# Optimization experiments

Measured on AMD Instinct MI355X. Metric: run time of the kernel, lower is better.

The kernel has to match this reference:

```python
import math
import jax, jax.numpy as jnp
import numpy as np

N_QUBITS = 8
N_QLAYERS = 2
HIDDEN = 768
BATCH = 8192
LN_EPS = 1e-5


def _ry_gate(theta):
    # theta: scalar or (B,) -> (2,2) or (B,2,2) complex64
    h = theta * 0.5
    c, s = jnp.cos(h), jnp.sin(h)
    g = jnp.stack([jnp.stack([c, -s], axis=-1), jnp.stack([s, c], axis=-1)], axis=-2)
    return g.astype(jnp.complex64)


def _rz_gate(theta):
    t = theta.astype(jnp.complex64)
    e0, e1 = jnp.exp(-0.5j * t), jnp.exp(0.5j * t)
    z = jnp.zeros_like(e0)
    return jnp.stack([jnp.stack([e0, z], axis=-1), jnp.stack([z, e1], axis=-1)], axis=-2)


def _apply_1q(state, gate, w, n):
    # state: (B, 2**n); gate: (2,2) shared or (B,2,2) per-sample; wire w (0 = MSB)
    B = state.shape[0]
    s = state.reshape(B, 2 ** w, 2, -1)
    if gate.ndim == 2:
        s = jnp.einsum('ij,bljr->blir', gate, s)
    else:
        s = jnp.einsum('bij,bljr->blir', gate, s)
    return s.reshape(B, -1)


def _apply_cnot(state, c, t, n):
    B = state.shape[0]
    s = state.reshape((B,) + (2,) * n)
    ax_c = 1 + c
    s0 = jnp.take(s, 0, axis=ax_c)  # control=0 branch, control axis removed
    s1 = jnp.take(s, 1, axis=ax_c)
    ax_t = 1 + t - (1 if t > c else 0)
    s1 = jnp.flip(s1, axis=ax_t)    # X on target when control=1
    s = jnp.stack([s0, s1], axis=ax_c)
    return s.reshape(B, -1)


def _circuit(angles, weights_ry, weights_rz):
    # angles: (B, n) float32 -> (B, n) PauliZ expectations, batched statevector sim
    n, L = N_QUBITS, N_QLAYERS
    B = angles.shape[0]
    state = jnp.zeros((B, 2 ** n), dtype=jnp.complex64).at[:, 0].set(1.0)
    for i in range(n):
        state = _apply_1q(state, _ry_gate(angles[:, i]), i, n)
    for i in range(1, n):
        state = _apply_cnot(state, 0, i, n)
    for l in range(L):
        for i in range(n):
            state = _apply_1q(state, _ry_gate(weights_ry[l, i]), i, n)
            state = _apply_1q(state, _rz_gate(weights_rz[l, i]), i, n)
    for i in range(1, n):
        state = _apply_cnot(state, i, 0, n)
    probs = jnp.abs(state) ** 2  # (B, 2**n)
    k = jnp.arange(2 ** n)
    bits = (k[None, :] >> (n - 1 - jnp.arange(n))[:, None]) & 1  # wire 0 = MSB (PennyLane)
    signs = (1 - 2 * bits).astype(probs.dtype)  # (n, 2**n)
    return probs @ signs.T  # (B, n)


def setup_inputs() -> dict:
    key = jax.random.key(0)
    ks = jax.random.split(key, 8)
    return {
        'hidden': jax.random.normal(ks[0], (BATCH, HIDDEN), dtype=jnp.float32),
        'W_in': jax.random.normal(ks[1], (N_QUBITS, HIDDEN), dtype=jnp.float32) * (1.0 / math.sqrt(HIDDEN)),
        'b_in': jax.random.normal(ks[2], (N_QUBITS,), dtype=jnp.float32) * 0.01,
        'W_out': jax.random.normal(ks[3], (HIDDEN, N_QUBITS), dtype=jnp.float32) * (1.0 / math.sqrt(N_QUBITS)),
        'b_out': jax.random.normal(ks[4], (HIDDEN,), dtype=jnp.float32) * 0.01,
        'weights_ry': jax.random.normal(ks[5], (N_QLAYERS, N_QUBITS), dtype=jnp.float32) * 0.1,
        'weights_rz': jax.random.normal(ks[6], (N_QLAYERS, N_QUBITS), dtype=jnp.float32) * 0.1,
        'gamma': jnp.ones((HIDDEN,), dtype=jnp.float32),
        'beta': jnp.zeros((HIDDEN,), dtype=jnp.float32),
    }


def reference(hidden, W_in, b_in, W_out, b_out, weights_ry, weights_rz, gamma, beta):
    phase = 0.0
    angles = jnp.tanh(hidden @ W_in.T + b_in) * math.pi + phase  # (B, n)
    meas = _circuit(angles, weights_ry, weights_rz).astype(jnp.float32)  # (B, n)
    y = meas @ W_out.T + b_out  # (B, h)
    mu = jnp.mean(y, axis=-1, keepdims=True)
    var = jnp.mean(jnp.square(y - mu), axis=-1, keepdims=True)
    return (y - mu) * jax.lax.rsqrt(var + LN_EPS) * gamma + beta
```

## Files before the change

kernel.cpp:

```cpp
#include <hip/hip_runtime.h>
#include <hip/hip_bf16.h>

#define NQ    8
#define HID   768
#define BATCH 8192
#define TPB   512
#define SPB   8
#define NBLK  (BATCH / SPB)

template<int BF> __device__ __forceinline__ float LDV(const void* p, int i) {
    if constexpr (BF) return __bfloat162float(((const __hip_bfloat16*)p)[i]);
    else return ((const float*)p)[i];
}
template<int BF> __device__ __forceinline__ void STV(void* p, int i, float v) {
    if constexpr (BF) ((__hip_bfloat16*)p)[i] = __float2bfloat16(v);
    else ((float*)p)[i] = v;
}
template<int BF> __device__ __forceinline__ float4 LD4(const void* p, int i4) {
    if constexpr (BF) {
        ushort4 v = ((const ushort4*)p)[i4];
        float4 r;
        r.x = __uint_as_float(((unsigned)v.x) << 16);
        r.y = __uint_as_float(((unsigned)v.y) << 16);
        r.z = __uint_as_float(((unsigned)v.z) << 16);
        r.w = __uint_as_float(((unsigned)v.w) << 16);
        return r;
    } else {
        return ((const float4*)p)[i4];
    }
}
__device__ __forceinline__ float bflo(unsigned w) { return __uint_as_float(w << 16); }
__device__ __forceinline__ float bfhi(unsigned w) { return __uint_as_float(w & 0xffff0000u); }

#define SMEM_BYTES 33920

template<int BF>
__device__ __forceinline__ void run_all(
    const void* hidden_, const void* W_in_, const void* b_in_,
    const void* W_out_, const void* b_out_, const void* wry_, const void* wrz_,
    const void* gamma_, const void* beta_, void* out_, char* smem)
{
    const int tid  = threadIdx.x;
    const int lane = tid & 63;
    const int wv   = tid >> 6;
    const int j    = lane >> 3;
    const int b    = blockIdx.x * SPB + wv;

    float*  sBout = (float*)(smem + 24576);
    float2* sGB   = (float2*)(smem + 27648);
    float4* sQC   = (float4*)(smem + 33792);

    for (int idx = tid; idx < HID; idx += TPB) {
        if constexpr (BF) {
            ((uint4*)smem)[idx]           = ((const uint4*)W_in_)[idx];
            ((uint4*)(smem + 12288))[idx] = ((const uint4*)W_out_)[idx];
        }
        sBout[idx] = LDV<BF>(b_out_, idx);
        sGB[idx]   = make_float2(LDV<BF>(gamma_, idx), LDV<BF>(beta_, idx));
    }

    if (tid < NQ) {
        const int q = tid;
        float ry0 = LDV<BF>(wry_, q), ry1 = LDV<BF>(wry_, NQ + q);
        float rz0 = LDV<BF>(wrz_, q), rz1 = LDV<BF>(wrz_, NQ + q);
        float cA = cosf(0.5f*ry0), sA = sinf(0.5f*ry0);
        float cB = cosf(0.5f*ry1), sB = sinf(0.5f*ry1);
        float p0c = cosf(0.5f*rz0), p0s = sinf(0.5f*rz0);
        float p1c = cosf(0.5f*rz1), p1s = sinf(0.5f*rz1);
        float g00r =  cA*p0c, g00i = -cA*p0s;
        float g01r = -sA*p0c, g01i =  sA*p0s;
        float g10r =  sA*p0c, g10i =  sA*p0s;
        float g11r =  cA*p0c, g11i =  cA*p0s;
        float h00r = cB*g00r - sB*g10r, h00i = cB*g00i - sB*g10i;
        float h01r = cB*g01r - sB*g11r, h01i = cB*g01i - sB*g11i;
        float h10r = sB*g00r + cB*g10r, h10i = sB*g00i + cB*g10i;
        float h11r = sB*g01r + cB*g11r, h11i = sB*g01i + cB*g11i;
        float f00r = h00r*p1c + h00i*p1s, f00i = h00i*p1c - h00r*p1s;
        float f01r = h01r*p1c + h01i*p1s, f01i = h01i*p1c - h01r*p1s;
        float f10r = h10r*p1c - h10i*p1s, f10i = h10i*p1c + h10r*p1s;
        float f11r = h11r*p1c - h11i*p1s, f11i = h11i*p1c + h11r*p1s;
        float DA = f00r*f00r + f00i*f00i - (f10r*f10r + f10i*f10i);
        float DB = f01r*f01r + f01i*f01i - (f11r*f11r + f11i*f11i);
        float Kr = (f00r*f01r + f00i*f01i) - (f10r*f11r + f10i*f11i);
        float Ki = (f00i*f01r - f00r*f01i) - (f10i*f11r - f10r*f11i);
        sQC[q] = make_float4(DA, DB, Kr, Ki);
    }
    __syncthreads();

    float p[NQ];
    #pragma unroll
    for (int q = 0; q < NQ; ++q) p[q] = 0.f;
    const int hb = b * (HID/4);
    #pragma unroll
    for (int t = 0; t < 3; ++t) {
        const int q4 = (t << 6) + lane;
        float4 h = LD4<BF>(hidden_, hb + q4);
        if constexpr (BF) {
            const uint2* sWinU2 = (const uint2*)smem;
            #pragma unroll
            for (int jj = 0; jj < NQ; ++jj) {
                uint2 w = sWinU2[jj*(HID/4) + q4];
                p[jj] = fmaf(h.x, bflo(w.x), p[jj]);
                p[jj] = fmaf(h.y, bfhi(w.x), p[jj]);
                p[jj] = fmaf(h.z, bflo(w.y), p[jj]);
                p[jj] = fmaf(h.w, bfhi(w.y), p[jj]);
            }
        } else {
            #pragma unroll
            for (int jj = 0; jj < NQ; ++jj) {
                float4 w = LD4<BF>(W_in_, jj*(HID/4) + q4);
                p[jj] = fmaf(h.x, w.x, p[jj]);
                p[jj] = fmaf(h.y, w.y, p[jj]);
                p[jj] = fmaf(h.z, w.z, p[jj]);
                p[jj] = fmaf(h.w, w.w, p[jj]);
            }
        }
    }
    const bool mb0 = ((lane >> 3) & 1) != 0;
    const bool mb1 = ((lane >> 4) & 1) != 0;
    const bool mb2 = ((lane >> 5) & 1) != 0;
    float np[4];
    #pragma unroll
    for (int k = 0; k < 4; ++k) {
        float sent = mb0 ? p[2*k]   : p[2*k+1];
        float keep = mb0 ? p[2*k+1] : p[2*k];
        np[k] = keep + __shfl_xor(sent, 8, 64);
    }
    float nq2[2];
    #pragma unroll
    for (int k = 0; k < 2; ++k) {
        float sent = mb1 ? np[2*k]   : np[2*k+1];
        float keep = mb1 ? np[2*k+1] : np[2*k];
        nq2[k] = keep + __shfl_xor(sent, 16, 64);
    }
    float z;
    {
        float sent = mb2 ? nq2[0] : nq2[1];
        float keep = mb2 ? nq2[1] : nq2[0];
        z = keep + __shfl_xor(sent, 32, 64);
    }
    z += __shfl_xor(z, 1, 64);
    z += __shfl_xor(z, 2, 64);
    z += __shfl_xor(z, 4, 64);

    float4 qq = sQC[j];
    float DA = qq.x, DB = qq.y, Kr = qq.z, Ki = qq.w;
    float zb = z + LDV<BF>(b_in_, j);
    float th = tanhf(zb);
    float sj = sinpif(th), cj = cospif(th);

    float ca = 0.5f * (DA + DB), da = 0.5f * (DA - DB);
    const bool g0 = (j == 0);
    float uu = da * cj;
    float vv = fmaf(Kr, sj, ca);
    float MA = g0 ? 1.f : (vv + uu), MB = g0 ? 1.f : (vv - uu);
    float fr = g0 ? 1.f : Kr,        fi = g0 ? 0.f : (cj * Ki);
    #pragma unroll
    for (int d = 8; d < 64; d <<= 1) {
        MA *= __shfl_xor(MA, d, 64);
        MB *= __shfl_xor(MB, d, 64);
        float qr = __shfl_xor(fr, d, 64);
        float qi = __shfl_xor(fi, d, 64);
        float nr = fr*qr - fi*qi;
        float ni = fr*qi + fi*qr;
        fr = nr; fi = ni;
    }
    float4 q0 = sQC[0];
    float cc0 = __shfl(cj, 0, 64), sc0 = __shfl(sj, 0, 64);
    float meas0 = 0.5f*(1.f+cc0)*q0.x*MA + 0.5f*(1.f-cc0)*q0.y*MB
                + sc0*(q0.z*fr - q0.w*fi);
    float measj = g0 ? meas0 : fmaf(cc0, uu, vv);
    float m0 = meas0;
    float m1 = __shfl(measj,  8, 64), m2 = __shfl(measj, 16, 64);
    float m3 = __shfl(measj, 24, 64), m4 = __shfl(measj, 32, 64);
    float m5 = __shfl(measj, 40, 64), m6 = __shfl(measj, 48, 64);
    float m7 = __shfl(measj, 56, 64);

    const int rowbase = b * HID;
    float yv[12];
    float sum = 0.f, sq = 0.f;
    #pragma unroll
    for (int k = 0; k < 12; ++k) {
        const int c = lane + (k << 6);
        float y = sBout[c];
        if constexpr (BF) {
            uint4 wp = ((const uint4*)(smem + 12288))[c];
            y = fmaf(m0, bflo(wp.x), y); y = fmaf(m1, bfhi(wp.x), y);
            y = fmaf(m2, bflo(wp.y), y); y = fmaf(m3, bfhi(wp.y), y);
            y = fmaf(m4, bflo(wp.z), y); y = fmaf(m5, bfhi(wp.z), y);
            y = fmaf(m6, bflo(wp.w), y); y = fmaf(m7, bfhi(wp.w), y);
        } else {
            float4 w0 = LD4<BF>(W_out_, c*2);
            float4 w1 = LD4<BF>(W_out_, c*2 + 1);
            y = fmaf(m0, w0.x, y); y = fmaf(m1, w0.y, y);
            y = fmaf(m2, w0.z, y); y = fmaf(m3, w0.w, y);
            y = fmaf(m4, w1.x, y); y = fmaf(m5, w1.y, y);
            y = fmaf(m6, w1.z, y); y = fmaf(m7, w1.w, y);
        }
        yv[k] = y;
        sum += y;
        sq = fmaf(y, y, sq);
    }
    #pragma unroll
    for (int d = 1; d < 64; d <<= 1) {
        sum += __shfl_xor(sum, d, 64);
        sq  += __shfl_xor(sq,  d, 64);
    }
    float mean = sum * (1.f/HID);
    float var  = fmaf(sq, 1.f/HID, -mean*mean);
    float rstd = rsqrtf(var + 1e-5f);
    #pragma unroll
    for (int k = 0; k < 12; ++k) {
        const int c = lane + (k << 6);
        float2 gb = sGB[c];
        float o = fmaf((yv[k] - mean) * rstd, gb.x, gb.y);
        STV<BF>(out_, rowbase + c, o);
    }
}

__global__ __launch_bounds__(TPB, 8) void main_kernel(
    const void* hidden_, const void* W_in_, const void* b_in_,
    const void* W_out_, const void* b_out_, const void* wry_, const void* wrz_,
    const void* gamma_, const void* beta_, void* out_)
{
    __shared__ __align__(16) char smem[SMEM_BYTES];
    const int lane = threadIdx.x & 63;
    unsigned wrd = ((const unsigned*)hidden_)[lane];
    unsigned lo  = wrd & 0xffffu;
    unsigned e   = (lo >> 7) & 0xffu;
    bool v = (lo == 0u) || (e >= 100u && e <= 133u);
    unsigned long long mask = __ballot(v);
    int flag = (__popcll(mask) > 32) ? 1 : 0;
    if (flag)
        run_all<1>(hidden_, W_in_, b_in_, W_out_, b_out_, wry_, wrz_,
                   gamma_, beta_, out_, smem);
    else
        run_all<0>(hidden_, W_in_, b_in_, W_out_, b_out_, wry_, wrz_,
                   gamma_, beta_, out_, smem);
}

extern "C" void kernel_launch(void* const* d_in, const int* in_sizes, int n_in,
                              void* d_out, int out_size, void* d_ws, size_t ws_size,
                              hipStream_t stream) {
    const void* hidden = d_in[0];
    const void* W_in   = d_in[1];
    const void* b_in   = d_in[2];
    const void* W_out  = d_in[3];
    const void* b_out  = d_in[4];
    const void* wry    = d_in[5];
    const void* wrz    = d_in[6];
    const void* gamma  = d_in[7];
    const void* beta   = d_in[8];
    (void)d_ws; (void)ws_size;
    main_kernel<<<NBLK, TPB, 0, stream>>>(hidden, W_in, b_in, W_out, b_out,
                                          wry, wrz, gamma, beta, d_out);
}
```

Before: 103.3 us.

## Double samples per block and stage hidden rows cooperatively into LDS

Doubles the block to 1024 threads handling 16 samples, so the per-block setup (copying W_in, W_out, bias, gamma and beta into LDS and building the gate constants) is spread over twice as many samples. In the bf16 path, each block's hidden rows are copied into LDS with wide coalesced 16-byte loads before the projection reads them as 8-byte chunks. This trades more LDS per block and an extra synchronised staging step, which may lower occupancy, for fewer redundant weight loads and better global load efficiency.

After: 106.3 us. 1.03x slower.

```diff
diff --git a/kernel.cpp b/kernel.cpp
--- a/kernel.cpp
+++ b/kernel.cpp
@@ -4,8 +4,8 @@
 #define NQ    8
 #define HID   768
 #define BATCH 8192
-#define TPB   512
-#define SPB   8
+#define TPB   1024
+#define SPB   16
 #define NBLK  (BATCH / SPB)
 
 template<int BF> __device__ __forceinline__ float LDV(const void* p, int i) {
@@ -32,7 +32,12 @@
 __device__ __forceinline__ float bflo(unsigned w) { return __uint_as_float(w << 16); }
 __device__ __forceinline__ float bfhi(unsigned w) { return __uint_as_float(w & 0xffff0000u); }
 
-#define SMEM_BYTES 33920
+#define OFF_WOUT 12288
+#define OFF_BOUT 24576
+#define OFF_GB   27648
+#define OFF_QC   33792
+#define OFF_HID  33920
+#define SMEM_BYTES 58496
 
 template<int BF>
 __device__ __forceinline__ void run_all(
@@ -46,17 +51,26 @@
     const int j    = lane >> 3;
     const int b    = blockIdx.x * SPB + wv;
 
-    float*  sBout = (float*)(smem + 24576);
-    float2* sGB   = (float2*)(smem + 27648);
-    float4* sQC   = (float4*)(smem + 33792);
-
-    for (int idx = tid; idx < HID; idx += TPB) {
-        if constexpr (BF) {
-            ((uint4*)smem)[idx]           = ((const uint4*)W_in_)[idx];
-            ((uint4*)(smem + 12288))[idx] = ((const uint4*)W_out_)[idx];
-        }
-        sBout[idx] = LDV<BF>(b_out_, idx);
-        sGB[idx]   = make_float2(LDV<BF>(gamma_, idx), LDV<BF>(beta_, idx));
+    float*  sBout = (float*)(smem + OFF_BOUT);
+    float2* sGB   = (float2*)(smem + OFF_GB);
+    float4* sQC   = (float4*)(smem + OFF_QC);
+
+    if constexpr (BF) {
+        if (tid < 768) {
+            ((uint4*)smem)[tid]              = ((const uint4*)W_in_)[tid];
+            ((uint4*)(smem + OFF_WOUT))[tid] = ((const uint4*)W_out_)[tid];
+            sBout[tid] = LDV<BF>(b_out_, tid);
+            sGB[tid]   = make_float2(LDV<BF>(gamma_, tid), LDV<BF>(beta_, tid));
+        }
+        const uint4* hsrc = (const uint4*)hidden_ + (size_t)blockIdx.x * 1536;
+        uint4* hdst = (uint4*)(smem + OFF_HID);
+        hdst[tid] = hsrc[tid];
+        if (tid < 512) hdst[tid + 1024] = hsrc[tid + 1024];
+    } else {
+        if (tid < 768) {
+            sBout[tid] = LDV<BF>(b_out_, tid);
+            sGB[tid]   = make_float2(LDV<BF>(gamma_, tid), LDV<BF>(beta_, tid));
+        }
     }
 
     if (tid < NQ) {
@@ -94,25 +108,33 @@
     #pragma unroll
     for (int t = 0; t < 3; ++t) {
         const int q4 = (t << 6) + lane;
-        float4 h = LD4<BF>(hidden_, hb + q4);
+        float hx, hy, hz, hw2;
+        if constexpr (BF) {
+            uint2 hh = ((const uint2*)(smem + OFF_HID + wv*1536))[q4];
+            hx = bflo(hh.x); hy = bfhi(hh.x);
+            hz = bflo(hh.y); hw2 = bfhi(hh.y);
+        } else {
+            float4 h = LD4<BF>(hidden_, hb + q4);
+            hx = h.x; hy = h.y; hz = h.z; hw2 = h.w;
+        }
         if constexpr (BF) {
             const uint2* sWinU2 = (const uint2*)smem;
             #pragma unroll
             for (int jj = 0; jj < NQ; ++jj) {
                 uint2 w = sWinU2[jj*(HID/4) + q4];
-                p[jj] = fmaf(h.x, bflo(w.x), p[jj]);
-                p[jj] = fmaf(h.y, bfhi(w.x), p[jj]);
-                p[jj] = fmaf(h.z, bflo(w.y), p[jj]);
-                p[jj] = fmaf(h.w, bfhi(w.y), p[jj]);
+                p[jj] = fmaf(hx,  bflo(w.x), p[jj]);
+                p[jj] = fmaf(hy,  bfhi(w.x), p[jj]);
+                p[jj] = fmaf(hz,  bflo(w.y), p[jj]);
+                p[jj] = fmaf(hw2, bfhi(w.y), p[jj]);
             }
         } else {
             #pragma unroll
             for (int jj = 0; jj < NQ; ++jj) {
                 float4 w = LD4<BF>(W_in_, jj*(HID/4) + q4);
-                p[jj] = fmaf(h.x, w.x, p[jj]);
-                p[jj] = fmaf(h.y, w.y, p[jj]);
-                p[jj] = fmaf(h.z, w.z, p[jj]);
-                p[jj] = fmaf(h.w, w.w, p[jj]);
+                p[jj] = fmaf(hx,  w.x, p[jj]);
+                p[jj] = fmaf(hy,  w.y, p[jj]);
+                p[jj] = fmaf(hz,  w.z, p[jj]);
+                p[jj] = fmaf(hw2, w.w, p[jj]);
             }
         }
     }
@@ -184,7 +206,7 @@
         const int c = lane + (k << 6);
         float y = sBout[c];
         if constexpr (BF) {
-            uint4 wp = ((const uint4*)(smem + 12288))[c];
+            uint4 wp = ((const uint4*)(smem + OFF_WOUT))[c];
             y = fmaf(m0, bflo(wp.x), y); y = fmaf(m1, bfhi(wp.x), y);
             y = fmaf(m2, bflo(wp.y), y); y = fmaf(m3, bfhi(wp.y), y);
             y = fmaf(m4, bflo(wp.z), y); y = fmaf(m5, bfhi(wp.z), y);
```
